# Kernel tuning notes

Measured on AMD Instinct MI355X. Metric: run time of the kernel, lower is better.

The kernel has to match this reference:

```python
import jax, jax.numpy as jnp
import numpy as np

D_MODEL = 1024
N_HEADS = 16
D_HEAD = D_MODEL // N_HEADS  # 64
SCALE = 1.0 / float(np.sqrt(D_HEAD))


def setup_inputs() -> dict:
    key = jax.random.key(0)
    kx, kq, kk, kv, ko = jax.random.split(key, 5)
    B, L = 1, 4096
    x = jax.random.normal(kx, (B, L, D_MODEL), dtype=jnp.float32)
    init = 0.02  # small init so softmax isn't saturated
    Wq = jax.random.normal(kq, (D_MODEL, D_MODEL), dtype=jnp.float32) * init
    Wk = jax.random.normal(kk, (D_MODEL, D_MODEL), dtype=jnp.float32) * init
    Wv = jax.random.normal(kv, (D_MODEL, D_MODEL), dtype=jnp.float32) * init
    Wo = jax.random.normal(ko, (D_MODEL, D_MODEL), dtype=jnp.float32) * init
    return {"x": x, "Wq": Wq, "Wk": Wk, "Wv": Wv, "Wo": Wo}


def reference(x, Wq, Wk, Wv, Wo):
    # x: [B, L, d_model]; torch Linear (no bias): y = x @ W.T
    B, L, _ = x.shape

    def split_heads(t):  # [B, L, d_model] -> [B, H, L, Dh]
        return t.reshape(B, L, N_HEADS, D_HEAD).transpose(0, 2, 1, 3)

    q = split_heads(x @ Wq.T)
    k = split_heads(x @ Wk.T)
    v = split_heads(x @ Wv.T)

    # Full (non-flash) attention: explicit [B, H, L, L] scores (causal=False, eval dropout=0)
    scores = jnp.einsum("bhld,bhmd->bhlm", q, k) * SCALE
    attn = jax.nn.softmax(scores, axis=-1)
    out = jnp.einsum("bhlm,bhmd->bhld", attn, v)

    out = out.transpose(0, 2, 1, 3).reshape(B, L, D_MODEL)
    return out @ Wo.T
```

## Files before the change

kernel.cpp:

```cpp
#include <hip/hip_runtime.h>

typedef _Float16 f16_t;
typedef __fp16 fp16x2 __attribute__((ext_vector_type(2)));
typedef _Float16 f16x2 __attribute__((ext_vector_type(2)));
typedef _Float16 f16x4 __attribute__((ext_vector_type(4)));
typedef _Float16 f16x8 __attribute__((ext_vector_type(8)));
typedef float f32x4 __attribute__((ext_vector_type(4)));

#define D_MODEL 1024
#define LSEQ 4096
#define NH 16
#define DH 64
#define QSCALE 0.18033688011112042f

#define GLDS16(g, l)                                                     \
    __builtin_amdgcn_global_load_lds(                                    \
        (const __attribute__((address_space(1))) void*)(g),              \
        (__attribute__((address_space(3))) void*)(l), 16, 0, 0)

#define WAIT_VM(n) asm volatile("s_waitcnt vmcnt(" #n ")" ::: "memory")

__global__ __launch_bounds__(256) void cvt_x(const float* __restrict__ in,
                                             f16_t* __restrict__ out, int n) {
    int i = (blockIdx.x * 256 + threadIdx.x) * 4;
    if (i + 3 < n) {
        float4 v = *(const float4*)&in[i];
        alignas(8) f16_t o4[4] = {(f16_t)v.x, (f16_t)v.y, (f16_t)v.z, (f16_t)v.w};
        *(uint2*)&out[i] = *(const uint2*)o4;
    }
}

__global__ __launch_bounds__(256) void cvt_w4(const float* __restrict__ w0,
                                              const float* __restrict__ w1,
                                              const float* __restrict__ w2,
                                              const float* __restrict__ w3,
                                              f16_t* __restrict__ out) {
    const int q = blockIdx.y;
    const float* src = (q == 0) ? w0 : (q == 1) ? w1 : (q == 2) ? w2 : w3;
    const float scale = (q == 0) ? QSCALE : 1.f;
    int i = (blockIdx.x * 256 + threadIdx.x) * 4;
    float4 v = *(const float4*)&src[i];
    alignas(8) f16_t o4[4] = {(f16_t)(v.x * scale), (f16_t)(v.y * scale),
                              (f16_t)(v.z * scale), (f16_t)(v.w * scale)};
    *(uint2*)&out[(size_t)q * (D_MODEL * D_MODEL) + i] = *(const uint2*)o4;
}

__global__ __launch_bounds__(256, 3) void gemm_f16(const f16_t* __restrict__ A,
                                                   const f16_t* __restrict__ B,
                                                   void* __restrict__ Cout,
                                                   int M, int N, int K, int mode) {
    __shared__ alignas(16) f16_t As[3][128 * 32];
    __shared__ alignas(16) f16_t Bs[3][128 * 32];

    const int tid  = threadIdx.x;
    const int wave = tid >> 6;
    const int lane = tid & 63;
    const int quad = lane >> 4;
    const int l16  = lane & 15;
    const int wm = (wave & 1) * 64;
    const int wn = (wave >> 1) * 64;
    const int bm = blockIdx.x * 128;
    const int bn = blockIdx.y * 128;

    f32x4 acc[4][4] = {};
    const int nk = K / 32;

    auto stage = [&](int kt, int b) {
        const int c0 = wave * 2;
        GLDS16(&A[(size_t)(bm + c0 * 16 + l16) * K + kt * 32 + quad * 8],
               &As[b][c0 * 512]);
        GLDS16(&A[(size_t)(bm + (c0 + 1) * 16 + l16) * K + kt * 32 + quad * 8],
               &As[b][(c0 + 1) * 512]);
        GLDS16(&B[(size_t)(bn + c0 * 16 + l16) * K + kt * 32 + quad * 8],
               &Bs[b][c0 * 512]);
        GLDS16(&B[(size_t)(bn + (c0 + 1) * 16 + l16) * K + kt * 32 + quad * 8],
               &Bs[b][(c0 + 1) * 512]);
    };

    stage(0, 0);
    stage(1, 1);
    for (int kt = 0; kt < nk; ++kt) {
        const int cb = kt % 3;
        if (kt < nk - 1) WAIT_VM(4);
        else             WAIT_VM(0);
        __syncthreads();
        if (kt + 2 < nk) stage(kt + 2, (kt + 2) % 3);

        f16x8 af[4], bfr[4];
#pragma unroll
        for (int mt = 0; mt < 4; ++mt)
            af[mt] = *(const f16x8*)&As[cb][((wm >> 4) + mt) * 512 + lane * 8];
#pragma unroll
        for (int nt = 0; nt < 4; ++nt)
            bfr[nt] = *(const f16x8*)&Bs[cb][((wn >> 4) + nt) * 512 + lane * 8];
#pragma unroll
        for (int mt = 0; mt < 4; ++mt)
#pragma unroll
            for (int nt = 0; nt < 4; ++nt)
                acc[mt][nt] = __builtin_amdgcn_mfma_f32_16x16x32_f16(
                    bfr[nt], af[mt], acc[mt][nt], 0, 0, 0);
    }

#pragma unroll
    for (int mt = 0; mt < 4; ++mt)
#pragma unroll
        for (int nt = 0; nt < 4; ++nt) {
            int row = bm + wm + mt * 16 + l16;
            int col = bn + wn + nt * 16 + quad * 4;
            if (mode == 0) {
                f16x4 p = {(f16_t)acc[mt][nt][0], (f16_t)acc[mt][nt][1],
                           (f16_t)acc[mt][nt][2], (f16_t)acc[mt][nt][3]};
                *(f16x4*)&((f16_t*)Cout)[((size_t)(col >> 6) * M + row) * 64 +
                                         (col & 63)] = p;
            } else {
                *(f32x4*)&((float*)Cout)[(size_t)row * N + col] = acc[mt][nt];
            }
        }
}

__global__ __launch_bounds__(256) void transpose_v(const f16_t* __restrict__ vh,
                                                   f16_t* __restrict__ v4) {
    __shared__ f16_t Ts[64][72];
    const int t = threadIdx.x;
    const int lt = blockIdx.x;
    const int head = blockIdx.y;

#pragma unroll
    for (int i = 0; i < 2; ++i) {
        int idx = t + i * 256;
        int row = idx >> 3, part = idx & 7;
        *(uint4*)&Ts[row][part * 8] =
            *(const uint4*)&vh[((size_t)head * LSEQ + lt * 64 + row) * DH + part * 8];
    }
    __syncthreads();

    const int c   = t >> 4;
    const int dt  = c >> 2, kb = c & 3;
    const int km2 = (t & 15) >> 2;
    const int dl2 = t & 3;
    alignas(16) f16_t buf[16];
#pragma unroll
    for (int i = 0; i < 16; ++i) {
        int j = i & 3, dd = i >> 2;
        buf[i] = Ts[kb * 16 + km2 * 4 + j][dt * 16 + dl2 * 4 + dd];
    }
    f16_t* dst = v4 + (size_t)head * (LSEQ * DH) + lt * 4096 + c * 256 + (t & 15) * 16;
    *(uint4*)&dst[0] = *(const uint4*)&buf[0];
    *(uint4*)&dst[8] = *(const uint4*)&buf[8];
}

__global__ __launch_bounds__(512, 2) void attn_kernel(const f16_t* __restrict__ qh,
                                                      const f16_t* __restrict__ kh,
                                                      const f16_t* __restrict__ v4,
                                                      f16_t* __restrict__ ao) {
    __shared__ alignas(16) f16_t smem[32768];
    __shared__ alignas(16) float lscr[16 * 64];
    f16_t* KsB = smem;
    f16_t* VsB = smem + 16384;

    const int tid  = threadIdx.x;
    const int wave = tid >> 6;
    const int lane = tid & 63;
    const int quad = lane >> 4;
    const int l16  = lane & 15;
    const int wq   = wave & 3;
    const int kha  = wave >> 2;

    const int id = blockIdx.x;
    const int head = id & 15;
    const int qrow0 = (id >> 4) * 256 + wq * 64;

    const f16_t* Q  = qh + (size_t)head * LSEQ * DH;
    const f16_t* K  = kh + (size_t)head * LSEQ * DH;
    const f16_t* V4 = v4 + (size_t)head * (LSEQ * DH);

    f16x8 qf[4][2];
#pragma unroll
    for (int qt = 0; qt < 4; ++qt)
#pragma unroll
        for (int kc = 0; kc < 2; ++kc)
            qf[qt][kc] = *(const f16x8*)
                &Q[(size_t)(qrow0 + qt * 16 + l16) * DH + kc * 32 + quad * 8];

    f32x4 o[4][4] = {};
    float lp[4] = {0.f, 0.f, 0.f, 0.f};

    auto stage = [&](int kt, int b) {
        f16_t* ks = KsB + (kha * 2 + b) * 4096;
        f16_t* vs = VsB + (kha * 2 + b) * 4096;
        const int ktg = kha * 32 + kt;
#pragma unroll
        for (int jj = 0; jj < 2; ++jj) {
            const int j = wq * 2 + jj;
            GLDS16(&K[(size_t)(ktg * 64 + wq * 16 + l16) * DH + jj * 32 + quad * 8],
                   &ks[j * 512]);
            GLDS16(&V4[(size_t)ktg * 4096 + wq * 1024 + jj * 512 + lane * 8],
                   &vs[wq * 1024 + jj * 512]);
        }
    };

    const int NT = LSEQ / 2 / 64;
    stage(0, 0);
    for (int kt = 0; kt < NT; ++kt) {
        const int cb = kt & 1;
        WAIT_VM(0);
        __syncthreads();
        if (kt + 1 < NT) stage(kt + 1, cb ^ 1);

        const f16_t* ks = KsB + (kha * 2 + cb) * 4096;
        const f16_t* vs = VsB + (kha * 2 + cb) * 4096;

#pragma unroll
        for (int mt = 0; mt < 4; ++mt) {
            f16x8 kf0 = *(const f16x8*)&ks[(mt * 2 + 0) * 512 + lane * 8];
            f16x8 kf1 = *(const f16x8*)&ks[(mt * 2 + 1) * 512 + lane * 8];

            f32x4 s[4] = {};
#pragma unroll
            for (int qt = 0; qt < 4; ++qt) {
                s[qt] = __builtin_amdgcn_mfma_f32_16x16x32_f16(kf0, qf[qt][0],
                                                               s[qt], 0, 0, 0);
                s[qt] = __builtin_amdgcn_mfma_f32_16x16x32_f16(kf1, qf[qt][1],
                                                               s[qt], 0, 0, 0);
            }

            f16x4 vfd[4];
#pragma unroll
            for (int dt = 0; dt < 4; ++dt)
                vfd[dt] = *(const f16x4*)&vs[(dt * 4 + mt) * 256 + lane * 4];

#pragma unroll
            for (int qt = 0; qt < 4; ++qt) {
                float e0 = __builtin_amdgcn_exp2f(s[qt][0]);
                float e1 = __builtin_amdgcn_exp2f(s[qt][1]);
                float e2 = __builtin_amdgcn_exp2f(s[qt][2]);
                float e3 = __builtin_amdgcn_exp2f(s[qt][3]);
                lp[qt] += (e0 + e1) + (e2 + e3);
                fp16x2 p01 = __builtin_amdgcn_cvt_pkrtz(e0, e1);
                fp16x2 p23 = __builtin_amdgcn_cvt_pkrtz(e2, e3);
                f16x4 p = {__builtin_bit_cast(f16x2, p01)[0],
                           __builtin_bit_cast(f16x2, p01)[1],
                           __builtin_bit_cast(f16x2, p23)[0],
                           __builtin_bit_cast(f16x2, p23)[1]};
#pragma unroll
                for (int dt = 0; dt < 4; ++dt)
                    o[dt][qt] = __builtin_amdgcn_mfma_f32_16x16x16f16(
                        vfd[dt], p, o[dt][qt], 0, 0, 0);
            }
        }
    }

    __syncthreads();
    float* scr = (float*)smem;
    if (wave >= 4) {
#pragma unroll
        for (int dt = 0; dt < 4; ++dt)
#pragma unroll
            for (int qt = 0; qt < 4; ++qt)
                *(f32x4*)&scr[(((wave - 4) * 16 + dt * 4 + qt) * 64 + lane) * 4] =
                    o[dt][qt];
#pragma unroll
        for (int qt = 0; qt < 4; ++qt)
            lscr[((wave - 4) * 4 + qt) * 64 + lane] = lp[qt];
    }
    __syncthreads();
    if (wave < 4) {
#pragma unroll
        for (int dt = 0; dt < 4; ++dt)
#pragma unroll
            for (int qt = 0; qt < 4; ++qt)
                o[dt][qt] += *(const f32x4*)
                    &scr[((wave * 16 + dt * 4 + qt) * 64 + lane) * 4];
#pragma unroll
        for (int qt = 0; qt < 4; ++qt) {
            float t = lp[qt] + lscr[(wave * 4 + qt) * 64 + lane];
            t += __shfl_xor(t, 16, 64);
            t += __shfl_xor(t, 32, 64);
            lp[qt] = 1.f / t;
        }
#pragma unroll
        for (int dt = 0; dt < 4; ++dt)
#pragma unroll
            for (int qt = 0; qt < 4; ++qt) {
                f16x4 ov = {(f16_t)(o[dt][qt][0] * lp[qt]),
                            (f16_t)(o[dt][qt][1] * lp[qt]),
                            (f16_t)(o[dt][qt][2] * lp[qt]),
                            (f16_t)(o[dt][qt][3] * lp[qt])};
                int qrow = qrow0 + qt * 16 + l16;
                *(f16x4*)&ao[(size_t)qrow * D_MODEL + head * 64 + dt * 16 +
                             quad * 4] = ov;
            }
    }
}

extern "C" void kernel_launch(void* const* d_in, const int* in_sizes, int n_in,
                              void* d_out, int out_size, void* d_ws, size_t ws_size,
                              hipStream_t stream) {
    const float* x  = (const float*)d_in[0];
    const float* Wq = (const float*)d_in[1];
    const float* Wk = (const float*)d_in[2];
    const float* Wv = (const float*)d_in[3];
    const float* Wo = (const float*)d_in[4];

    f16_t* xb = (f16_t*)d_ws;
    f16_t* wq = xb + (size_t)LSEQ * D_MODEL;
    f16_t* wo = wq + (size_t)3 * D_MODEL * D_MODEL;
    f16_t* qh = wo + (size_t)D_MODEL * D_MODEL;
    f16_t* kh = qh + (size_t)LSEQ * D_MODEL;
    f16_t* vh = kh + (size_t)LSEQ * D_MODEL;
    f16_t* v4 = vh + (size_t)LSEQ * D_MODEL;
    f16_t* ao = v4 + (size_t)LSEQ * D_MODEL;

    const int nx = LSEQ * D_MODEL;
    cvt_x<<<nx / 1024, 256, 0, stream>>>(x, xb, nx);
    cvt_w4<<<dim3(D_MODEL * D_MODEL / 1024, 4), 256, 0, stream>>>(Wq, Wk, Wv, Wo, wq);

    gemm_f16<<<dim3(LSEQ / 128, 3 * D_MODEL / 128), 256, 0, stream>>>(
        xb, wq, qh, LSEQ, 3 * D_MODEL, D_MODEL, 0);

    transpose_v<<<dim3(LSEQ / 64, NH), 256, 0, stream>>>(vh, v4);

    attn_kernel<<<dim3((LSEQ / 256) * NH), 512, 0, stream>>>(qh, kh, v4, ao);

    gemm_f16<<<dim3(LSEQ / 128, D_MODEL / 128), 256, 0, stream>>>(
        ao, wo, d_out, LSEQ, D_MODEL, D_MODEL, 1);
}
```

Measured before the change: 259.1 us.

## Split attention keys four ways per block with 128-row query tiles

The attention kernel now gives each block 128 query rows (2 query-wave groups) and splits the key range four ways across waves, doubling the grid to 512 blocks. Double buffering of K/V in LDS is replaced by a single buffer with a sync before refilling, and launch bounds request 4 blocks per CU. The partial outputs and row sums are reduced in two LDS stages. This aims to raise occupancy and fill the GPU better, but gives up load/compute overlap and adds reduction cost and register pressure.

```diff
diff --git a/kernel.cpp b/kernel.cpp
--- a/kernel.cpp
+++ b/kernel.cpp
@@ -149,26 +149,26 @@
     *(uint4*)&dst[8] = *(const uint4*)&buf[8];
 }
 
-__global__ __launch_bounds__(512, 2) void attn_kernel(const f16_t* __restrict__ qh,
+__global__ __launch_bounds__(512, 4) void attn_kernel(const f16_t* __restrict__ qh,
                                                       const f16_t* __restrict__ kh,
                                                       const f16_t* __restrict__ v4,
                                                       f16_t* __restrict__ ao) {
     __shared__ alignas(16) f16_t smem[32768];
-    __shared__ alignas(16) float lscr[16 * 64];
-    f16_t* KsB = smem;
-    f16_t* VsB = smem + 16384;
+    __shared__ alignas(16) float lscr[8][4][64];
+    f16_t* Ks = smem;
+    f16_t* Vs = smem + 16384;
 
     const int tid  = threadIdx.x;
     const int wave = tid >> 6;
     const int lane = tid & 63;
     const int quad = lane >> 4;
     const int l16  = lane & 15;
-    const int wq   = wave & 3;
-    const int kha  = wave >> 2;
+    const int wq   = wave & 1;
+    const int kq   = wave >> 1;
 
     const int id = blockIdx.x;
-    const int head = id & 15;
-    const int qrow0 = (id >> 4) * 256 + wq * 64;
+    const int head = (id & 7) * 2 + ((id >> 3) & 1);
+    const int qrow0 = (id >> 4) * 128 + wq * 64;
 
     const f16_t* Q  = qh + (size_t)head * LSEQ * DH;
     const f16_t* K  = kh + (size_t)head * LSEQ * DH;
@@ -185,30 +185,27 @@
     f32x4 o[4][4] = {};
     float lp[4] = {0.f, 0.f, 0.f, 0.f};
 
-    auto stage = [&](int kt, int b) {
-        f16_t* ks = KsB + (kha * 2 + b) * 4096;
-        f16_t* vs = VsB + (kha * 2 + b) * 4096;
-        const int ktg = kha * 32 + kt;
-#pragma unroll
-        for (int jj = 0; jj < 2; ++jj) {
-            const int j = wq * 2 + jj;
-            GLDS16(&K[(size_t)(ktg * 64 + wq * 16 + l16) * DH + jj * 32 + quad * 8],
+    auto stage = [&](int kt) {
+        f16_t* ks = Ks + kq * 4096;
+        f16_t* vs = Vs + kq * 4096;
+        const int ktg = kq * 16 + kt;
+#pragma unroll
+        for (int jj = 0; jj < 4; ++jj) {
+            const int j = wq * 4 + jj, mt = j >> 1, kc = j & 1;
+            GLDS16(&K[(size_t)(ktg * 64 + mt * 16 + l16) * DH + kc * 32 + quad * 8],
                    &ks[j * 512]);
-            GLDS16(&V4[(size_t)ktg * 4096 + wq * 1024 + jj * 512 + lane * 8],
-                   &vs[wq * 1024 + jj * 512]);
+            GLDS16(&V4[(size_t)ktg * 4096 + wq * 2048 + jj * 512 + lane * 8],
+                   &vs[wq * 2048 + jj * 512]);
         }
     };
 
-    const int NT = LSEQ / 2 / 64;
-    stage(0, 0);
+    const int NT = 16;
+    stage(0);
     for (int kt = 0; kt < NT; ++kt) {
-        const int cb = kt & 1;
         WAIT_VM(0);
         __syncthreads();
-        if (kt + 1 < NT) stage(kt + 1, cb ^ 1);
-
-        const f16_t* ks = KsB + (kha * 2 + cb) * 4096;
-        const f16_t* vs = VsB + (kha * 2 + cb) * 4096;
+        const f16_t* ks = Ks + kq * 4096;
+        const f16_t* vs = Vs + kq * 4096;
 
 #pragma unroll
         for (int mt = 0; mt < 4; ++mt) {
@@ -248,32 +245,57 @@
                         vfd[dt], p, o[dt][qt], 0, 0, 0);
             }
         }
-    }
-
+        __syncthreads();
+        if (kt + 1 < NT) stage(kt + 1);
+    }
+
+    float* scr = (float*)smem;
+    if (kq >= 2) {
+        const int slot = wq * 2 + (kq - 2);
+#pragma unroll
+        for (int dt = 0; dt < 4; ++dt)
+#pragma unroll
+            for (int qt = 0; qt < 4; ++qt)
+                *(f32x4*)&scr[slot * 4096 + ((dt * 4 + qt) * 64 + lane) * 4] =
+                    o[dt][qt];
+#pragma unroll
+        for (int qt = 0; qt < 4; ++qt) lscr[wave][qt][lane] = lp[qt];
+    }
     __syncthreads();
-    float* scr = (float*)smem;
-    if (wave >= 4) {
-#pragma unroll
-        for (int dt = 0; dt < 4; ++dt)
-#pragma unroll
-            for (int qt = 0; qt < 4; ++qt)
-                *(f32x4*)&scr[(((wave - 4) * 16 + dt * 4 + qt) * 64 + lane) * 4] =
-                    o[dt][qt];
-#pragma unroll
-        for (int qt = 0; qt < 4; ++qt)
-            lscr[((wave - 4) * 4 + qt) * 64 + lane] = lp[qt];
-    }
-    __syncthreads();
-    if (wave < 4) {
+    if (kq < 2) {
+        const int slot = wq * 2 + kq;
 #pragma unroll
         for (int dt = 0; dt < 4; ++dt)
 #pragma unroll
             for (int qt = 0; qt < 4; ++qt)
                 o[dt][qt] += *(const f32x4*)
-                    &scr[((wave * 16 + dt * 4 + qt) * 64 + lane) * 4];
+                    &scr[slot * 4096 + ((dt * 4 + qt) * 64 + lane) * 4];
+#pragma unroll
+        for (int qt = 0; qt < 4; ++qt)
+            lp[qt] += lscr[(kq + 2) * 2 + wq][qt][lane];
+    }
+    __syncthreads();
+    if (kq == 1) {
+#pragma unroll
+        for (int dt = 0; dt < 4; ++dt)
+#pragma unroll
+            for (int qt = 0; qt < 4; ++qt)
+                *(f32x4*)&scr[wq * 4096 + ((dt * 4 + qt) * 64 + lane) * 4] =
+                    o[dt][qt];
+#pragma unroll
+        for (int qt = 0; qt < 4; ++qt) lscr[wave][qt][lane] = lp[qt];
+    }
+    __syncthreads();
+    if (kq == 0) {
+#pragma unroll
+        for (int dt = 0; dt < 4; ++dt)
+#pragma unroll
+            for (int qt = 0; qt < 4; ++qt)
+                o[dt][qt] += *(const f32x4*)
+                    &scr[wq * 4096 + ((dt * 4 + qt) * 64 + lane) * 4];
 #pragma unroll
         for (int qt = 0; qt < 4; ++qt) {
-            float t = lp[qt] + lscr[(wave * 4 + qt) * 64 + lane];
+            float t = lp[qt] + lscr[2 + wq][qt][lane];
             t += __shfl_xor(t, 16, 64);
             t += __shfl_xor(t, 32, 64);
             lp[qt] = 1.f / t;
@@ -320,7 +342,7 @@
 
     transpose_v<<<dim3(LSEQ / 64, NH), 256, 0, stream>>>(vh, v4);
 
-    attn_kernel<<<dim3((LSEQ / 256) * NH), 512, 0, stream>>>(qh, kh, v4, ao);
+    attn_kernel<<<dim3((LSEQ / 128) * NH), 512, 0, stream>>>(qh, kh, v4, ao);
 
     gemm_f16<<<dim3(LSEQ / 128, D_MODEL / 128), 256, 0, stream>>>(
         ao, wo, d_out, LSEQ, D_MODEL, D_MODEL, 1);
```

Measured after the change: 957.9 us. +269.6%, slower.
